# Kernel tuning notes

Measured on AMD Instinct MI355X. Metric: run time of the kernel, lower is better.

Reference implementation:

```python
import jax, jax.numpy as jnp
import numpy as np

N = 50000        # nodes
E = 400000       # edges (avg degree 8)
F_IN = 128       # num_features
HID = 64         # hidden_channels
H = 4            # num_heads
D = HID // H     # headc = 16
C = 16           # num_classes
K_HOPS = 3
ALPHA = 0.1
CST = 1e-5


def setup_inputs() -> dict:
    key = jax.random.key(0)
    ks = jax.random.split(key, 16)
    s = 0.05
    x = jax.random.normal(ks[0], (N, F_IN), dtype=jnp.float32)
    edge_index = jax.random.randint(ks[1], (2, E), 0, N, dtype=jnp.int64)
    Wi = jax.random.normal(ks[2], (F_IN, HID), dtype=jnp.float32) * s
    bi = jnp.zeros((HID,), dtype=jnp.float32)
    Wq = jax.random.normal(ks[3], (HID, H * D), dtype=jnp.float32) * s
    bq = jnp.zeros((H * D,), dtype=jnp.float32)
    Wk = jax.random.normal(ks[4], (HID, H * D), dtype=jnp.float32) * s
    bk = jnp.zeros((H * D,), dtype=jnp.float32)
    Wv = jax.random.normal(ks[5], (HID, H * C), dtype=jnp.float32) * s
    bv = jnp.zeros((H * C,), dtype=jnp.float32)
    Wo = jax.random.normal(ks[6], (H * C, C), dtype=jnp.float32) * s
    bo = jnp.zeros((C,), dtype=jnp.float32)
    # hopwise/temp init as in the torch module (ind_gamma=True, gamma_softmax=True)
    hw = ALPHA * (1.0 - ALPHA) ** np.arange(K_HOPS + 1)
    hw[-1] = (1.0 - ALPHA) ** K_HOPS
    hopwise = jnp.asarray(hw, dtype=jnp.float32)
    temp = jax.random.uniform(ks[7], (H, K_HOPS + 1), dtype=jnp.float32)
    return {"x": x, "edge_index": edge_index, "Wi": Wi, "bi": bi, "Wq": Wq,
            "bq": bq, "Wk": Wk, "bk": bk, "Wv": Wv, "bv": bv, "Wo": Wo,
            "bo": bo, "hopwise": hopwise, "temp": temp}


def reference(x, edge_index, Wi, bi, Wq, bq, Wk, bk, Wv, bv, Wo, bo, hopwise, temp):
    # dropout p=0 (inference); input transform + relu
    h = jax.nn.relu(x @ Wi + bi)                       # (N, HID)
    Q = (1.0 + jax.nn.elu(h @ Wq + bq)).reshape(N, H, D)
    Kt = (1.0 + jax.nn.elu(h @ Wk + bk)).reshape(N, H, D)
    V = (h @ Wv + bv).reshape(N, H, C)
    M = jnp.einsum('nhi,nhj->nhij', Kt, V)             # (N, H, D, C)
    hidden = V * temp[:, 0][None, :, None]             # hop-0 term
    # NB: torch F.softmax(temp, dim=-2) normalizes over the HEAD axis
    layerwise = jax.nn.softmax(temp, axis=0)           # (H, K+1)
    src, dst = edge_index[0], edge_index[1]
    for hop in range(K_HOPS):
        M = jax.ops.segment_sum(M[src], dst, num_segments=N)
        Kt = jax.ops.segment_sum(Kt[src], dst, num_segments=N)
        Hm = jnp.einsum('nhi,nhij->nhj', Q, M)         # (N, H, C)
        den = jnp.einsum('nhi,nhi->nh', Q, Kt)[..., None] + CST
        gamma = hopwise[hop + 1] * layerwise[:, hop + 1][:, None]  # (H, 1)
        hidden = hidden + gamma * (Hm / den)
    # multi_concat=True path
    out = hidden.reshape(N, H * C) @ Wo + bo           # (N, C)
    return out
```

## Files before the change

### kernel.cpp

```cpp
#include <hip/hip_runtime.h>
#include <math.h>

#define F_IN 128
#define HID  64
#define NH   4
#define DD   16
#define CC   16
#define CSTE 1e-5f

typedef _Float16 h2     __attribute__((ext_vector_type(2)));
typedef float    f2     __attribute__((ext_vector_type(2)));
typedef short    short8 __attribute__((ext_vector_type(8)));
typedef float    f4v    __attribute__((ext_vector_type(4)));

#define WIT_LD 136
#define W2T_LD 72
#define H_LD   72

__device__ __forceinline__ unsigned short bf16r(float f) {
    unsigned int u = __builtin_bit_cast(unsigned int, f);
    unsigned int r = (u + 0x7FFFu + ((u >> 16) & 1u)) >> 16;
    return (unsigned short)r;
}

__device__ __forceinline__ int uni(int v) {
    return __builtin_amdgcn_readfirstlane(v);
}

__device__ __forceinline__ float fp8_to_f32(unsigned int b) {
    f2 v = __builtin_amdgcn_cvt_pk_f32_fp8((int)b, false);
    return v.x;
}
__device__ __forceinline__ f2 fp8x2_to_f32(unsigned int w) {
    return __builtin_amdgcn_cvt_pk_f32_fp8((int)w, false);
}
__device__ __forceinline__ unsigned char f32_to_fp8(float f) {
    int w = __builtin_amdgcn_cvt_pk_fp8_f32(f, f, 0, false);
    return (unsigned char)(w & 0xff);
}

__device__ __forceinline__ float fp4_dec1(unsigned int n) {
    unsigned int e = (n >> 1) & 3u, m = n & 1u;
    float mag = (e == 0) ? 0.5f * (float)m
                         : (float)(1u << (e - 1)) * (1.0f + 0.5f * (float)m);
    return (n & 8u) ? -mag : mag;
}
__device__ __forceinline__ unsigned int fp4_enc1(float f) {
    unsigned int s = (f < 0.f) ? 8u : 0u;
    float a = fabsf(f);
    unsigned int m;
    if      (a < 0.25f) m = 0u;
    else if (a < 0.75f) m = 1u;
    else if (a < 1.25f) m = 2u;
    else if (a < 1.75f) m = 3u;
    else if (a < 2.5f)  m = 4u;
    else if (a < 3.5f)  m = 5u;
    else if (a < 5.0f)  m = 6u;
    else                m = 7u;
    return s | m;
}

#if __has_builtin(__builtin_amdgcn_cvt_scalef32_pk_f32_fp4) && __has_builtin(__builtin_amdgcn_cvt_scalef32_pk_fp4_f32)
#define HAS_FP4 1
#endif

__device__ __forceinline__ void fp4x16_dec2(uint2 w, f2* v) {
#ifdef HAS_FP4
    v[0] = __builtin_amdgcn_cvt_scalef32_pk_f32_fp4(w.x, 1.0f, 0);
    v[1] = __builtin_amdgcn_cvt_scalef32_pk_f32_fp4(w.x, 1.0f, 1);
    v[2] = __builtin_amdgcn_cvt_scalef32_pk_f32_fp4(w.x, 1.0f, 2);
    v[3] = __builtin_amdgcn_cvt_scalef32_pk_f32_fp4(w.x, 1.0f, 3);
    v[4] = __builtin_amdgcn_cvt_scalef32_pk_f32_fp4(w.y, 1.0f, 0);
    v[5] = __builtin_amdgcn_cvt_scalef32_pk_f32_fp4(w.y, 1.0f, 1);
    v[6] = __builtin_amdgcn_cvt_scalef32_pk_f32_fp4(w.y, 1.0f, 2);
    v[7] = __builtin_amdgcn_cvt_scalef32_pk_f32_fp4(w.y, 1.0f, 3);
#else
    #pragma unroll
    for (int j = 0; j < 4; ++j) {
        v[j].x     = fp4_dec1((w.x >> (8 * j)) & 0xFu);
        v[j].y     = fp4_dec1((w.x >> (8 * j + 4)) & 0xFu);
        v[4 + j].x = fp4_dec1((w.y >> (8 * j)) & 0xFu);
        v[4 + j].y = fp4_dec1((w.y >> (8 * j + 4)) & 0xFu);
    }
#endif
}

__device__ __forceinline__ uint2 fp4x16_enc(const float* v) {
#ifdef HAS_FP4
    unsigned int a = 0u, b = 0u;
    a = __builtin_amdgcn_cvt_scalef32_pk_fp4_f32(a, v[0],  v[1],  1.0f, 0);
    a = __builtin_amdgcn_cvt_scalef32_pk_fp4_f32(a, v[2],  v[3],  1.0f, 1);
    a = __builtin_amdgcn_cvt_scalef32_pk_fp4_f32(a, v[4],  v[5],  1.0f, 2);
    a = __builtin_amdgcn_cvt_scalef32_pk_fp4_f32(a, v[6],  v[7],  1.0f, 3);
    b = __builtin_amdgcn_cvt_scalef32_pk_fp4_f32(b, v[8],  v[9],  1.0f, 0);
    b = __builtin_amdgcn_cvt_scalef32_pk_fp4_f32(b, v[10], v[11], 1.0f, 1);
    b = __builtin_amdgcn_cvt_scalef32_pk_fp4_f32(b, v[12], v[13], 1.0f, 2);
    b = __builtin_amdgcn_cvt_scalef32_pk_fp4_f32(b, v[14], v[15], 1.0f, 3);
    return {a, b};
#else
    unsigned int a = 0u, b = 0u;
    #pragma unroll
    for (int j = 0; j < 8; ++j) {
        a |= fp4_enc1(v[j])     << (4 * j);
        b |= fp4_enc1(v[8 + j]) << (4 * j);
    }
    return {a, b};
#endif
}

__device__ __forceinline__ void store_m_row(
    uint2* __restrict__ Mout, unsigned short* __restrict__ SKout,
    int node, int lane, const float* u, float kacc)
{
    float rm = 0.f;
    #pragma unroll
    for (int j = 0; j < 16; ++j) rm = fmaxf(rm, fabsf(u[j]));
    unsigned char s8 = f32_to_fp8(rm * (1.0f / 6.0f));
    float se = fp8_to_f32((unsigned int)s8);
    float invs = (se > 0.f) ? (1.0f / se) : 0.f;
    float tq[16];
    #pragma unroll
    for (int j = 0; j < 16; ++j) tq[j] = u[j] * invs;
    Mout[(size_t)node * 64 + lane] = fp4x16_enc(tq);
    SKout[(size_t)node * 64 + lane] =
        (unsigned short)((unsigned short)s8 | ((unsigned short)f32_to_fp8(kacc) << 8));
}

__device__ __forceinline__ float gamma_for(const float* __restrict__ temp,
                                           const float* __restrict__ hopwise,
                                           int h, int hop) {
    float t0 = temp[0 * 4 + hop], t1 = temp[1 * 4 + hop];
    float t2 = temp[2 * 4 + hop], t3 = temp[3 * 4 + hop];
    float mx = fmaxf(fmaxf(t0, t1), fmaxf(t2, t3));
    float e0 = __expf(t0 - mx), e1 = __expf(t1 - mx);
    float e2 = __expf(t2 - mx), e3 = __expf(t3 - mx);
    float ssum = e0 + e1 + e2 + e3;
    float eh = (h == 0) ? e0 : (h == 1) ? e1 : (h == 2) ? e2 : e3;
    return hopwise[hop] * eh / ssum;
}

__device__ __forceinline__ void reduce_scatter16(float* u, int p) {
    #pragma unroll
    for (int k = 0; k < 4; ++k) {
        const int m = 1 << k;
        bool bit = (p >> k) & 1;
        const int n = 8 >> k;
        #pragma unroll
        for (int j = 0; j < n; ++j) {
            float give = bit ? u[2 * j]     : u[2 * j + 1];
            float keep = bit ? u[2 * j + 1] : u[2 * j];
            float got  = __shfl_xor(give, m, 64);
            u[j] = keep + got;
        }
    }
}

__device__ __forceinline__ float den16(float qd, float kacc) {
    float kq = qd * kacc;
    kq += __shfl_xor(kq, 1, 64);
    kq += __shfl_xor(kq, 2, 64);
    kq += __shfl_xor(kq, 4, 64);
    kq += __shfl_xor(kq, 8, 64);
    return kq + CSTE;
}

__device__ __forceinline__ void acc_edge23(f2* u2, float& kacc,
                                           uint2 w, unsigned int skraw) {
    f2 sk = fp8x2_to_f32(skraw);
    kacc += sk.y;
    f2 v[8];
    fp4x16_dec2(w, v);
    f2 s = {sk.x, sk.x};
    #pragma unroll
    for (int j = 0; j < 8; ++j) u2[j] = s * v[j] + u2[j];
}

__device__ __forceinline__ void acc_edge1(h2* u16, float& kacc,
                                          uint4 a0, uint4 a1, unsigned int kraw) {
    float kk = fp8_to_f32(kraw);
    kacc += kk;
    _Float16 kh = (_Float16)kk;
    h2 k2 = {kh, kh};
    const unsigned int aw[8] = {a0.x, a0.y, a0.z, a0.w, a1.x, a1.y, a1.z, a1.w};
    #pragma unroll
    for (int j = 0; j < 8; ++j)
        u16[j] += k2 * __builtin_bit_cast(h2, aw[j]);
}

__global__ __launch_bounds__(1024) void scan_a(const int* __restrict__ deg,
                                               int* __restrict__ offsets,
                                               int* __restrict__ bsum, int N) {
    __shared__ int wsum[16], woff[16];
    int lane = threadIdx.x & 63, w = threadIdx.x >> 6;
    int i0 = blockIdx.x * 4096 + (int)threadIdx.x * 4;
    int d0 = (i0 + 0 < N) ? deg[i0 + 0] : 0;
    int d1 = (i0 + 1 < N) ? deg[i0 + 1] : 0;
    int d2 = (i0 + 2 < N) ? deg[i0 + 2] : 0;
    int d3 = (i0 + 3 < N) ? deg[i0 + 3] : 0;
    int tsum = d0 + d1 + d2 + d3;
    int incl = tsum;
    #pragma unroll
    for (int m = 1; m < 64; m <<= 1) {
        int t = __shfl_up(incl, m, 64);
        if (lane >= m) incl += t;
    }
    if (lane == 63) wsum[w] = incl;
    __syncthreads();
    if (threadIdx.x == 0) {
        int r = 0;
        for (int k = 0; k < 16; ++k) { int t = wsum[k]; woff[k] = r; r += t; }
        bsum[blockIdx.x] = r;
    }
    __syncthreads();
    int excl = woff[w] + incl - tsum;
    if (i0 + 0 < N) offsets[i0 + 0] = excl;
    if (i0 + 1 < N) offsets[i0 + 1] = excl + d0;
    if (i0 + 2 < N) offsets[i0 + 2] = excl + d0 + d1;
    if (i0 + 3 < N) offsets[i0 + 3] = excl + d0 + d1 + d2;
}

__global__ void scan_c(int* __restrict__ offsets, const int* __restrict__ bsum,
                       int nb, int N) {
    int i = blockIdx.x * blockDim.x + threadIdx.x;
    if (i < N) {
        int bkt = i >> 12;
        int base = 0;
        for (int b = 0; b < bkt; ++b) base += bsum[b];
        offsets[i] += base;
    }
    if (i == 0) {
        int tot = 0;
        for (int b = 0; b < nb; ++b) tot += bsum[b];
        offsets[N] = tot;
    }
}

__global__ void scatter_kernel(const int* __restrict__ ei, const int* __restrict__ offsets,
                               int* __restrict__ cursor, int* __restrict__ csr, int E) {
    int e = blockIdx.x * blockDim.x + threadIdx.x;
    if (e < E) {
        int src = ei[e];
        int dst = ei[E + e];
        int pos = atomicAdd(&cursor[dst], 1);
        csr[offsets[dst] + pos] = src;
    }
}

__global__ __launch_bounds__(256) void qkv_count(
    const float* __restrict__ x,
    const float* __restrict__ Wi, const float* __restrict__ bi,
    const float* __restrict__ Wq, const float* __restrict__ bq,
    const float* __restrict__ Wk, const float* __restrict__ bk,
    const float* __restrict__ Wv, const float* __restrict__ bv,
    float* __restrict__ Q, unsigned char* __restrict__ K0,
    _Float16* __restrict__ Vh,
    const int* __restrict__ ei, int* __restrict__ deg,
    int E, int qb, int N)
{
    __shared__ unsigned short wit[64 * WIT_LD];
    __shared__ unsigned short w2t[192 * W2T_LD];
    __shared__ unsigned short hlds[64 * H_LD];
    if ((int)blockIdx.x >= qb) {
        int e = ((int)blockIdx.x - qb) * 256 + (int)threadIdx.x;
        if (e < E) atomicAdd(&deg[ei[E + e]], 1);
        return;
    }
    int t = threadIdx.x;
    #pragma unroll
    for (int i = 0; i < 32; ++i) {
        int g = t + i * 256;
        wit[(g & 63) * WIT_LD + (g >> 6)] = bf16r(Wi[g]);
    }
    #pragma unroll
    for (int i = 0; i < 16; ++i) {
        int g = t + i * 256;
        int k = g >> 6, n = g & 63;
        w2t[(n      ) * W2T_LD + k] = bf16r(Wq[g]);
        w2t[(n +  64) * W2T_LD + k] = bf16r(Wk[g]);
        w2t[(n + 128) * W2T_LD + k] = bf16r(Wv[g]);
    }
    __syncthreads();

    int lane = t & 63, w = t >> 6;
    int p = lane & 15, quad = lane >> 4;
    int mbase = blockIdx.x * 64 + w * 16;

    short8 afrag[4];
    {
        int node = mbase + p;
        if (node >= N) node = N - 1;
        const float* xr = x + (size_t)node * F_IN + quad * 8;
        #pragma unroll
        for (int ks = 0; ks < 4; ++ks) {
            float4 a0 = *(const float4*)(xr + ks * 32);
            float4 a1 = *(const float4*)(xr + ks * 32 + 4);
            short8 f;
            f[0] = bf16r(a0.x); f[1] = bf16r(a0.y); f[2] = bf16r(a0.z); f[3] = bf16r(a0.w);
            f[4] = bf16r(a1.x); f[5] = bf16r(a1.y); f[6] = bf16r(a1.z); f[7] = bf16r(a1.w);
            afrag[ks] = f;
        }
    }
    #pragma unroll
    for (int nt = 0; nt < 4; ++nt) {
        f4v acc = {0.f, 0.f, 0.f, 0.f};
        #pragma unroll
        for (int ks = 0; ks < 4; ++ks) {
            short8 b = *(const short8*)&wit[(nt * 16 + p) * WIT_LD + ks * 32 + quad * 8];
            acc = __builtin_amdgcn_mfma_f32_16x16x32_bf16(afrag[ks], b, acc, 0, 0, 0);
        }
        float bb = bi[nt * 16 + p];
        #pragma unroll
        for (int r = 0; r < 4; ++r) {
            float hv = fmaxf(acc[r] + bb, 0.f);
            hlds[(w * 16 + quad * 4 + r) * H_LD + nt * 16 + p] = bf16r(hv);
        }
    }
    __syncthreads();

    short8 ha0 = *(const short8*)&hlds[(w * 16 + p) * H_LD + quad * 8];
    short8 ha1 = *(const short8*)&hlds[(w * 16 + p) * H_LD + 32 + quad * 8];
    int node_r = mbase + quad * 4;
    #pragma unroll
    for (int nt = 0; nt < 12; ++nt) {
        f4v acc = {0.f, 0.f, 0.f, 0.f};
        short8 b0 = *(const short8*)&w2t[(nt * 16 + p) * W2T_LD + quad * 8];
        short8 b1 = *(const short8*)&w2t[(nt * 16 + p) * W2T_LD + 32 + quad * 8];
        acc = __builtin_amdgcn_mfma_f32_16x16x32_bf16(ha0, b0, acc, 0, 0, 0);
        acc = __builtin_amdgcn_mfma_f32_16x16x32_bf16(ha1, b1, acc, 0, 0, 0);
        int col = nt * 16 + p;
        #pragma unroll
        for (int r = 0; r < 4; ++r) {
            int node = node_r + r;
            if (node >= N) continue;
            float v = acc[r];
            if (col < 64) {
                v += bq[col];
                Q[(size_t)node * 64 + col] = (v > 0.f) ? (1.f + v) : __expf(v);
            } else if (col < 128) {
                int c = col - 64;
                v += bk[c];
                float kv = (v > 0.f) ? (1.f + v) : __expf(v);
                K0[(size_t)node * 64 + c] = f32_to_fp8(kv);
            } else {
                int c = col - 128;
                v += bv[c];
                Vh[(size_t)node * 64 + c] = (_Float16)v;
            }
        }
    }
}


__global__ __launch_bounds__(256) void hop1_all(
    const float* __restrict__ Q, const unsigned char* __restrict__ K0,
    const _Float16* __restrict__ Vh,
    const int* __restrict__ offsets, const int* __restrict__ csr,
    const float* __restrict__ temp, const float* __restrict__ hopwise,
    uint2* __restrict__ M1, unsigned short* __restrict__ SK1,
    float* __restrict__ hidden, int N)
{
    int lane = threadIdx.x & 63;
    int h = lane >> 4;
    float gh  = gamma_for(temp, hopwise, h, 1);
    float g0  = temp[h * 4];
    int wid    = blockIdx.x * 4 + (threadIdx.x >> 6);
    int nwaves = gridDim.x * 4;

    for (int node = wid; node < N; node += nwaves) {
        float h0 = (float)Vh[(size_t)node * 64 + lane] * g0;
        float qd = Q[(size_t)node * 64 + lane];
        h2 u16[8];
        #pragma unroll
        for (int j = 0; j < 8; ++j) u16[j] = h2{(_Float16)0.f, (_Float16)0.f};
        float kacc = 0.f;
        int beg = uni(offsets[node]), end = uni(offsets[node + 1]);
        int t = beg;
        for (; t + 3 < end; t += 4) {
            int s0 = uni(csr[t]),     s1 = uni(csr[t + 1]);
            int s2 = uni(csr[t + 2]), s3 = uni(csr[t + 3]);
            const uint4* v0p = (const uint4*)(Vh + (size_t)s0 * 64 + h * 16);
            const uint4* v1p = (const uint4*)(Vh + (size_t)s1 * 64 + h * 16);
            const uint4* v2p = (const uint4*)(Vh + (size_t)s2 * 64 + h * 16);
            const uint4* v3p = (const uint4*)(Vh + (size_t)s3 * 64 + h * 16);
            uint4 a00 = v0p[0], a01 = v0p[1];
            uint4 a10 = v1p[0], a11 = v1p[1];
            uint4 a20 = v2p[0], a21 = v2p[1];
            uint4 a30 = v3p[0], a31 = v3p[1];
            unsigned char k0 = K0[(size_t)s0 * 64 + lane];
            unsigned char k1 = K0[(size_t)s1 * 64 + lane];
            unsigned char k2 = K0[(size_t)s2 * 64 + lane];
            unsigned char k3 = K0[(size_t)s3 * 64 + lane];
            acc_edge1(u16, kacc, a00, a01, k0);
            acc_edge1(u16, kacc, a10, a11, k1);
            acc_edge1(u16, kacc, a20, a21, k2);
            acc_edge1(u16, kacc, a30, a31, k3);
        }
        for (; t < end; ++t) {
            int s = uni(csr[t]);
            const uint4* vp = (const uint4*)(Vh + (size_t)s * 64 + h * 16);
            uint4 a0 = vp[0], a1 = vp[1];
            unsigned char kk = K0[(size_t)s * 64 + lane];
            acc_edge1(u16, kacc, a0, a1, kk);
        }
        float u[16];
        #pragma unroll
        for (int j = 0; j < 8; ++j) { u[2 * j] = (float)u16[j].x; u[2 * j + 1] = (float)u16[j].y; }
        store_m_row(M1, SK1, node, lane, u, kacc);
        #pragma unroll
        for (int j = 0; j < 16; ++j) u[j] *= qd;
        reduce_scatter16(u, lane & 15);
        float g = gh / den16(qd, kacc);
        hidden[(size_t)node * 64 + lane] = h0 + g * u[0];
    }
}

template<bool STORE>
__global__ __launch_bounds__(256) void hop23_all(
    const float* __restrict__ Q, const uint2* __restrict__ Mprev,
    const unsigned short* __restrict__ SKprev,
    const int* __restrict__ offsets, const int* __restrict__ csr,
    const float* __restrict__ temp, const float* __restrict__ hopwise,
    uint2* __restrict__ Mnext, unsigned short* __restrict__ SKnext,
    float* __restrict__ hidden,
    const float* __restrict__ Wo, const float* __restrict__ bo,
    float* __restrict__ out, int N, int hop)
{
    int lane = threadIdx.x & 63;
    float gh = gamma_for(temp, hopwise, lane >> 4, hop);
    int wid    = blockIdx.x * 4 + (threadIdx.x >> 6);
    int nwaves = gridDim.x * 4;

    for (int node = wid; node < N; node += nwaves) {
        float qd  = Q[(size_t)node * 64 + lane];
        float hv0 = STORE ? 0.f : hidden[(size_t)node * 64 + lane];
        f2 u2[8];
        #pragma unroll
        for (int j = 0; j < 8; ++j) u2[j] = f2{0.f, 0.f};
        float kacc = 0.f;
        int beg = uni(offsets[node]), end = uni(offsets[node + 1]);
        int t = beg;
        for (; t + 3 < end; t += 4) {
            int s0 = uni(csr[t]),     s1 = uni(csr[t + 1]);
            int s2 = uni(csr[t + 2]), s3 = uni(csr[t + 3]);
            uint2 w0 = Mprev[(size_t)s0 * 64 + lane];
            uint2 w1 = Mprev[(size_t)s1 * 64 + lane];
            uint2 w2 = Mprev[(size_t)s2 * 64 + lane];
            uint2 w3 = Mprev[(size_t)s3 * 64 + lane];
            unsigned short k0 = SKprev[(size_t)s0 * 64 + lane];
            unsigned short k1 = SKprev[(size_t)s1 * 64 + lane];
            unsigned short k2 = SKprev[(size_t)s2 * 64 + lane];
            unsigned short k3 = SKprev[(size_t)s3 * 64 + lane];
            acc_edge23(u2, kacc, w0, k0);
            acc_edge23(u2, kacc, w1, k1);
            acc_edge23(u2, kacc, w2, k2);
            acc_edge23(u2, kacc, w3, k3);
        }
        for (; t < end; ++t) {
            int sn = uni(csr[t]);
            uint2 w = Mprev[(size_t)sn * 64 + lane];
            unsigned short skr = SKprev[(size_t)sn * 64 + lane];
            acc_edge23(u2, kacc, w, skr);
        }
        float u[16];
        #pragma unroll
        for (int j = 0; j < 8; ++j) { u[2 * j] = u2[j].x; u[2 * j + 1] = u2[j].y; }
        if constexpr (STORE) store_m_row(Mnext, SKnext, node, lane, u, kacc);
        #pragma unroll
        for (int j = 0; j < 16; ++j) u[j] *= qd;
        reduce_scatter16(u, lane & 15);
        float g = gh / den16(qd, kacc);
        if constexpr (STORE) {
            hidden[(size_t)node * 64 + lane] += g * u[0];
        } else {
            float wrow[16];
            {
                const f4v* wp = (const f4v*)(Wo + (size_t)lane * 16);
                f4v a = wp[0], b = wp[1], c = wp[2], d = wp[3];
                wrow[0]=a[0]; wrow[1]=a[1]; wrow[2]=a[2]; wrow[3]=a[3];
                wrow[4]=b[0]; wrow[5]=b[1]; wrow[6]=b[2]; wrow[7]=b[3];
                wrow[8]=c[0]; wrow[9]=c[1]; wrow[10]=c[2]; wrow[11]=c[3];
                wrow[12]=d[0]; wrow[13]=d[1]; wrow[14]=d[2]; wrow[15]=d[3];
            }
            float hv = hv0 + g * u[0];
            float o[16];
            #pragma unroll
            for (int j = 0; j < 16; ++j) o[j] = hv * wrow[j];
            reduce_scatter16(o, lane & 15);
            float r = o[0];
            r += __shfl_xor(r, 16, 64);
            r += __shfl_xor(r, 32, 64);
            if (lane < 16) out[(size_t)node * 16 + lane] = r + bo[lane];
        }
    }
}

extern "C" void kernel_launch(void* const* d_in, const int* in_sizes, int n_in,
                              void* d_out, int out_size, void* d_ws, size_t ws_size,
                              hipStream_t stream) {
    const float* x       = (const float*)d_in[0];
    const int*   ei      = (const int*)  d_in[1];
    const float* Wi      = (const float*)d_in[2];
    const float* bi      = (const float*)d_in[3];
    const float* Wq      = (const float*)d_in[4];
    const float* bq      = (const float*)d_in[5];
    const float* Wk      = (const float*)d_in[6];
    const float* bk      = (const float*)d_in[7];
    const float* Wv      = (const float*)d_in[8];
    const float* bv      = (const float*)d_in[9];
    const float* Wo      = (const float*)d_in[10];
    const float* bo      = (const float*)d_in[11];
    const float* hopwise = (const float*)d_in[12];
    const float* temp    = (const float*)d_in[13];

    const int N = in_sizes[0] / F_IN;
    const int E = in_sizes[1] / 2;

    char* ws = (char*)d_ws;
    size_t off = 0;
    auto take = [&](size_t bytes) -> char* {
        char* p = ws + off;
        off += (bytes + 255) & ~(size_t)255;
        return p;
    };
    float*          Q      = (float*)take((size_t)N * 64 * 4);
    _Float16*       Vh     = (_Float16*)take((size_t)N * 64 * 2);
    float*          hidden = (float*)take((size_t)N * 64 * 4);
    unsigned char*  K0     = (unsigned char*)take((size_t)N * 64);
    unsigned short* SK1    = (unsigned short*)take((size_t)N * 64 * 2);
    unsigned short* SK2    = (unsigned short*)take((size_t)N * 64 * 2);
    int*            degcur = (int*)take((size_t)2 * N * 4);
    int*            offs   = (int*)take((size_t)(N + 1) * 4);
    int*            csr    = (int*)take((size_t)E * 4);
    int             nb     = (N + 4095) / 4096;
    int*            bsum   = (int*)take((size_t)nb * 4);
    uint2*          M1     = (uint2*)take((size_t)N * 512);
    uint2*          M2     = (uint2*)take((size_t)N * 512);

    int* deg    = degcur;
    int* cursor = degcur + N;

    hipMemsetAsync(degcur, 0, (size_t)2 * N * 4, stream);

    int eb = (E + 255) / 256;
    int qb = (N + 63) / 64;
    qkv_count<<<qb + eb, 256, 0, stream>>>(x, Wi, bi, Wq, bq, Wk, bk, Wv, bv,
                                           Q, K0, Vh,
                                           ei, deg, E, qb, N);
    scan_a<<<nb, 1024, 0, stream>>>(deg, offs, bsum, N);
    scan_c<<<(N + 255) / 256, 256, 0, stream>>>(offs, bsum, nb, N);
    scatter_kernel<<<eb, 256, 0, stream>>>(ei, offs, cursor, csr, E);

    int nwb = (N + 3) / 4;
    int pgrid = nwb < 2048 ? nwb : 2048;
    hop1_all<<<pgrid, 256, 0, stream>>>(Q, K0, Vh, offs, csr, temp, hopwise,
                                        M1, SK1, hidden, N);
    hop23_all<true ><<<pgrid, 256, 0, stream>>>(Q, M1, SK1, offs, csr, temp, hopwise,
                                                M2, SK2, hidden,
                                                (const float*)nullptr, (const float*)nullptr,
                                                (float*)nullptr, N, 2);
    hop23_all<false><<<pgrid, 256, 0, stream>>>(Q, M2, SK2, offs, csr, temp, hopwise,
                                                (uint2*)nullptr, (unsigned short*)nullptr,
                                                hidden, Wo, bo, (float*)d_out, N, 3);
}
```

Measured before the change: 295.6 us.

## Pack fp8 V and K into one interleaved row and use one-node-per-wave grids

The projection kernel now also writes V as fp8, packed with the fp8 K into a single 128-byte row per node. Hop 1 then gathers one contiguous row per neighbour instead of separate fp16 V and fp8 K rows, and accumulates in fp32. This cuts the bytes and cache lines touched in the gather. All three hop kernels also drop the grid-stride loop in favour of one wave per node with a full-size grid, trading loop overhead for more block launches. The cost is lower V precision in hop 1 (fp8 instead of fp16) and one extra store in the projection kernel.

```diff
diff --git a/kernel.cpp b/kernel.cpp
--- a/kernel.cpp
+++ b/kernel.cpp
@@ -33,6 +33,9 @@
 }
 __device__ __forceinline__ f2 fp8x2_to_f32(unsigned int w) {
     return __builtin_amdgcn_cvt_pk_f32_fp8((int)w, false);
+}
+__device__ __forceinline__ f2 fp8x2_to_f32_hi(unsigned int w) {
+    return __builtin_amdgcn_cvt_pk_f32_fp8((int)w, true);
 }
 __device__ __forceinline__ unsigned char f32_to_fp8(float f) {
     int w = __builtin_amdgcn_cvt_pk_fp8_f32(f, f, 0, false);
@@ -175,16 +178,18 @@
     for (int j = 0; j < 8; ++j) u2[j] = s * v[j] + u2[j];
 }
 
-__device__ __forceinline__ void acc_edge1(h2* u16, float& kacc,
-                                          uint4 a0, uint4 a1, unsigned int kraw) {
+__device__ __forceinline__ void acc_edge1(f2* u2, float& kacc,
+                                          uint4 vw, unsigned int kraw) {
     float kk = fp8_to_f32(kraw);
     kacc += kk;
-    _Float16 kh = (_Float16)kk;
-    h2 k2 = {kh, kh};
-    const unsigned int aw[8] = {a0.x, a0.y, a0.z, a0.w, a1.x, a1.y, a1.z, a1.w};
-    #pragma unroll
-    for (int j = 0; j < 8; ++j)
-        u16[j] += k2 * __builtin_bit_cast(h2, aw[j]);
+    f2 v[8];
+    v[0] = fp8x2_to_f32(vw.x);  v[1] = fp8x2_to_f32_hi(vw.x);
+    v[2] = fp8x2_to_f32(vw.y);  v[3] = fp8x2_to_f32_hi(vw.y);
+    v[4] = fp8x2_to_f32(vw.z);  v[5] = fp8x2_to_f32_hi(vw.z);
+    v[6] = fp8x2_to_f32(vw.w);  v[7] = fp8x2_to_f32_hi(vw.w);
+    f2 s = {kk, kk};
+    #pragma unroll
+    for (int j = 0; j < 8; ++j) u2[j] = s * v[j] + u2[j];
 }
 
 __global__ __launch_bounds__(1024) void scan_a(const int* __restrict__ deg,
@@ -252,7 +257,7 @@
     const float* __restrict__ Wq, const float* __restrict__ bq,
     const float* __restrict__ Wk, const float* __restrict__ bk,
     const float* __restrict__ Wv, const float* __restrict__ bv,
-    float* __restrict__ Q, unsigned char* __restrict__ K0,
+    float* __restrict__ Q, unsigned char* __restrict__ VKq,
     _Float16* __restrict__ Vh,
     const int* __restrict__ ei, int* __restrict__ deg,
     int E, int qb, int N)
@@ -340,11 +345,12 @@
                 int c = col - 64;
                 v += bk[c];
                 float kv = (v > 0.f) ? (1.f + v) : __expf(v);
-                K0[(size_t)node * 64 + c] = f32_to_fp8(kv);
+                VKq[(size_t)node * 128 + 64 + c] = f32_to_fp8(kv);
             } else {
                 int c = col - 128;
                 v += bv[c];
                 Vh[(size_t)node * 64 + c] = (_Float16)v;
+                VKq[(size_t)node * 128 + c] = f32_to_fp8(v);
             }
         }
     }
@@ -352,7 +358,7 @@
 
 
 __global__ __launch_bounds__(256) void hop1_all(
-    const float* __restrict__ Q, const unsigned char* __restrict__ K0,
+    const float* __restrict__ Q, const unsigned char* __restrict__ VKq,
     const _Float16* __restrict__ Vh,
     const int* __restrict__ offsets, const int* __restrict__ csr,
     const float* __restrict__ temp, const float* __restrict__ hopwise,
@@ -360,58 +366,54 @@
     float* __restrict__ hidden, int N)
 {
     int lane = threadIdx.x & 63;
+    int node = blockIdx.x * 4 + (threadIdx.x >> 6);
+    if (node >= N) return;
     int h = lane >> 4;
-    float gh  = gamma_for(temp, hopwise, h, 1);
-    float g0  = temp[h * 4];
-    int wid    = blockIdx.x * 4 + (threadIdx.x >> 6);
-    int nwaves = gridDim.x * 4;
-
-    for (int node = wid; node < N; node += nwaves) {
-        float h0 = (float)Vh[(size_t)node * 64 + lane] * g0;
-        float qd = Q[(size_t)node * 64 + lane];
-        h2 u16[8];
-        #pragma unroll
-        for (int j = 0; j < 8; ++j) u16[j] = h2{(_Float16)0.f, (_Float16)0.f};
-        float kacc = 0.f;
-        int beg = uni(offsets[node]), end = uni(offsets[node + 1]);
-        int t = beg;
-        for (; t + 3 < end; t += 4) {
-            int s0 = uni(csr[t]),     s1 = uni(csr[t + 1]);
-            int s2 = uni(csr[t + 2]), s3 = uni(csr[t + 3]);
-            const uint4* v0p = (const uint4*)(Vh + (size_t)s0 * 64 + h * 16);
-            const uint4* v1p = (const uint4*)(Vh + (size_t)s1 * 64 + h * 16);
-            const uint4* v2p = (const uint4*)(Vh + (size_t)s2 * 64 + h * 16);
-            const uint4* v3p = (const uint4*)(Vh + (size_t)s3 * 64 + h * 16);
-            uint4 a00 = v0p[0], a01 = v0p[1];
-            uint4 a10 = v1p[0], a11 = v1p[1];
-            uint4 a20 = v2p[0], a21 = v2p[1];
-            uint4 a30 = v3p[0], a31 = v3p[1];
-            unsigned char k0 = K0[(size_t)s0 * 64 + lane];
-            unsigned char k1 = K0[(size_t)s1 * 64 + lane];
-            unsigned char k2 = K0[(size_t)s2 * 64 + lane];
-            unsigned char k3 = K0[(size_t)s3 * 64 + lane];
-            acc_edge1(u16, kacc, a00, a01, k0);
-            acc_edge1(u16, kacc, a10, a11, k1);
-            acc_edge1(u16, kacc, a20, a21, k2);
-            acc_edge1(u16, kacc, a30, a31, k3);
-        }
-        for (; t < end; ++t) {
-            int s = uni(csr[t]);
-            const uint4* vp = (const uint4*)(Vh + (size_t)s * 64 + h * 16);
-            uint4 a0 = vp[0], a1 = vp[1];
-            unsigned char kk = K0[(size_t)s * 64 + lane];
-            acc_edge1(u16, kacc, a0, a1, kk);
-        }
-        float u[16];
-        #pragma unroll
-        for (int j = 0; j < 8; ++j) { u[2 * j] = (float)u16[j].x; u[2 * j + 1] = (float)u16[j].y; }
-        store_m_row(M1, SK1, node, lane, u, kacc);
-        #pragma unroll
-        for (int j = 0; j < 16; ++j) u[j] *= qd;
-        reduce_scatter16(u, lane & 15);
-        float g = gh / den16(qd, kacc);
-        hidden[(size_t)node * 64 + lane] = h0 + g * u[0];
-    }
+    float gh = gamma_for(temp, hopwise, h, 1);
+    float h0 = (float)Vh[(size_t)node * 64 + lane] * temp[h * 4];
+    float qd = Q[(size_t)node * 64 + lane];
+    f2 u2[8];
+    #pragma unroll
+    for (int j = 0; j < 8; ++j) u2[j] = f2{0.f, 0.f};
+    float kacc = 0.f;
+    int beg = uni(offsets[node]), end = uni(offsets[node + 1]);
+    int t = beg;
+    for (; t + 3 < end; t += 4) {
+        int s0 = uni(csr[t]),     s1 = uni(csr[t + 1]);
+        int s2 = uni(csr[t + 2]), s3 = uni(csr[t + 3]);
+        const unsigned char* b0 = VKq + (size_t)s0 * 128;
+        const unsigned char* b1 = VKq + (size_t)s1 * 128;
+        const unsigned char* b2 = VKq + (size_t)s2 * 128;
+        const unsigned char* b3 = VKq + (size_t)s3 * 128;
+        uint4 v0 = *(const uint4*)(b0 + h * 16);
+        uint4 v1 = *(const uint4*)(b1 + h * 16);
+        uint4 v2 = *(const uint4*)(b2 + h * 16);
+        uint4 v3 = *(const uint4*)(b3 + h * 16);
+        unsigned char k0 = b0[64 + lane];
+        unsigned char k1 = b1[64 + lane];
+        unsigned char k2 = b2[64 + lane];
+        unsigned char k3 = b3[64 + lane];
+        acc_edge1(u2, kacc, v0, k0);
+        acc_edge1(u2, kacc, v1, k1);
+        acc_edge1(u2, kacc, v2, k2);
+        acc_edge1(u2, kacc, v3, k3);
+    }
+    for (; t < end; ++t) {
+        int s = uni(csr[t]);
+        const unsigned char* b = VKq + (size_t)s * 128;
+        uint4 vw = *(const uint4*)(b + h * 16);
+        unsigned char kk = b[64 + lane];
+        acc_edge1(u2, kacc, vw, kk);
+    }
+    float u[16];
+    #pragma unroll
+    for (int j = 0; j < 8; ++j) { u[2 * j] = u2[j].x; u[2 * j + 1] = u2[j].y; }
+    store_m_row(M1, SK1, node, lane, u, kacc);
+    #pragma unroll
+    for (int j = 0; j < 16; ++j) u[j] *= qd;
+    reduce_scatter16(u, lane & 15);
+    float g = gh / den16(qd, kacc);
+    hidden[(size_t)node * 64 + lane] = h0 + g * u[0];
 }
 
 template<bool STORE>
@@ -426,71 +428,68 @@
     float* __restrict__ out, int N, int hop)
 {
     int lane = threadIdx.x & 63;
+    int node = blockIdx.x * 4 + (threadIdx.x >> 6);
+    if (node >= N) return;
     float gh = gamma_for(temp, hopwise, lane >> 4, hop);
-    int wid    = blockIdx.x * 4 + (threadIdx.x >> 6);
-    int nwaves = gridDim.x * 4;
-
-    for (int node = wid; node < N; node += nwaves) {
-        float qd  = Q[(size_t)node * 64 + lane];
-        float hv0 = STORE ? 0.f : hidden[(size_t)node * 64 + lane];
-        f2 u2[8];
+    float qd  = Q[(size_t)node * 64 + lane];
+    float hv0 = STORE ? 0.f : hidden[(size_t)node * 64 + lane];
+    f2 u2[8];
+    #pragma unroll
+    for (int j = 0; j < 8; ++j) u2[j] = f2{0.f, 0.f};
+    float kacc = 0.f;
+    int beg = uni(offsets[node]), end = uni(offsets[node + 1]);
+    int t = beg;
+    for (; t + 3 < end; t += 4) {
+        int s0 = uni(csr[t]),     s1 = uni(csr[t + 1]);
+        int s2 = uni(csr[t + 2]), s3 = uni(csr[t + 3]);
+        uint2 w0 = Mprev[(size_t)s0 * 64 + lane];
+        uint2 w1 = Mprev[(size_t)s1 * 64 + lane];
+        uint2 w2 = Mprev[(size_t)s2 * 64 + lane];
+        uint2 w3 = Mprev[(size_t)s3 * 64 + lane];
+        unsigned short k0 = SKprev[(size_t)s0 * 64 + lane];
+        unsigned short k1 = SKprev[(size_t)s1 * 64 + lane];
+        unsigned short k2 = SKprev[(size_t)s2 * 64 + lane];
+        unsigned short k3 = SKprev[(size_t)s3 * 64 + lane];
+        acc_edge23(u2, kacc, w0, k0);
+        acc_edge23(u2, kacc, w1, k1);
+        acc_edge23(u2, kacc, w2, k2);
+        acc_edge23(u2, kacc, w3, k3);
+    }
+    for (; t < end; ++t) {
+        int sn = uni(csr[t]);
+        uint2 w = Mprev[(size_t)sn * 64 + lane];
+        unsigned short skr = SKprev[(size_t)sn * 64 + lane];
+        acc_edge23(u2, kacc, w, skr);
+    }
+    float u[16];
+    #pragma unroll
+    for (int j = 0; j < 8; ++j) { u[2 * j] = u2[j].x; u[2 * j + 1] = u2[j].y; }
+    if constexpr (STORE) store_m_row(Mnext, SKnext, node, lane, u, kacc);
+    #pragma unroll
+    for (int j = 0; j < 16; ++j) u[j] *= qd;
+    reduce_scatter16(u, lane & 15);
+    float g = gh / den16(qd, kacc);
+    if constexpr (STORE) {
+        hidden[(size_t)node * 64 + lane] += g * u[0];
+    } else {
+        float wrow[16];
+        {
+            const f4v* wp = (const f4v*)(Wo + (size_t)lane * 16);
+            f4v a = wp[0], b = wp[1], c = wp[2], d = wp[3];
+            wrow[0]=a[0]; wrow[1]=a[1]; wrow[2]=a[2]; wrow[3]=a[3];
+            wrow[4]=b[0]; wrow[5]=b[1]; wrow[6]=b[2]; wrow[7]=b[3];
+            wrow[8]=c[0]; wrow[9]=c[1]; wrow[10]=c[2]; wrow[11]=c[3];
+            wrow[12]=d[0]; wrow[13]=d[1]; wrow[14]=d[2]; wrow[15]=d[3];
+        }
+        float hv = hv0 + g * u[0];
+        float o[16];
         #pragma unroll
-        for (int j = 0; j < 8; ++j) u2[j] = f2{0.f, 0.f};
-        float kacc = 0.f;
-        int beg = uni(offsets[node]), end = uni(offsets[node + 1]);
-        int t = beg;
-        for (; t + 3 < end; t += 4) {
-            int s0 = uni(csr[t]),     s1 = uni(csr[t + 1]);
-            int s2 = uni(csr[t + 2]), s3 = uni(csr[t + 3]);
-            uint2 w0 = Mprev[(size_t)s0 * 64 + lane];
-            uint2 w1 = Mprev[(size_t)s1 * 64 + lane];
-            uint2 w2 = Mprev[(size_t)s2 * 64 + lane];
-            uint2 w3 = Mprev[(size_t)s3 * 64 + lane];
-            unsigned short k0 = SKprev[(size_t)s0 * 64 + lane];
-            unsigned short k1 = SKprev[(size_t)s1 * 64 + lane];
-            unsigned short k2 = SKprev[(size_t)s2 * 64 + lane];
-            unsigned short k3 = SKprev[(size_t)s3 * 64 + lane];
-            acc_edge23(u2, kacc, w0, k0);
-            acc_edge23(u2, kacc, w1, k1);
-            acc_edge23(u2, kacc, w2, k2);
-            acc_edge23(u2, kacc, w3, k3);
-        }
-        for (; t < end; ++t) {
-            int sn = uni(csr[t]);
-            uint2 w = Mprev[(size_t)sn * 64 + lane];
-            unsigned short skr = SKprev[(size_t)sn * 64 + lane];
-            acc_edge23(u2, kacc, w, skr);
-        }
-        float u[16];
-        #pragma unroll
-        for (int j = 0; j < 8; ++j) { u[2 * j] = u2[j].x; u[2 * j + 1] = u2[j].y; }
-        if constexpr (STORE) store_m_row(Mnext, SKnext, node, lane, u, kacc);
-        #pragma unroll
-        for (int j = 0; j < 16; ++j) u[j] *= qd;
-        reduce_scatter16(u, lane & 15);
-        float g = gh / den16(qd, kacc);
-        if constexpr (STORE) {
-            hidden[(size_t)node * 64 + lane] += g * u[0];
-        } else {
-            float wrow[16];
-            {
-                const f4v* wp = (const f4v*)(Wo + (size_t)lane * 16);
-                f4v a = wp[0], b = wp[1], c = wp[2], d = wp[3];
-                wrow[0]=a[0]; wrow[1]=a[1]; wrow[2]=a[2]; wrow[3]=a[3];
-                wrow[4]=b[0]; wrow[5]=b[1]; wrow[6]=b[2]; wrow[7]=b[3];
-                wrow[8]=c[0]; wrow[9]=c[1]; wrow[10]=c[2]; wrow[11]=c[3];
-                wrow[12]=d[0]; wrow[13]=d[1]; wrow[14]=d[2]; wrow[15]=d[3];
-            }
-            float hv = hv0 + g * u[0];
-            float o[16];
-            #pragma unroll
-            for (int j = 0; j < 16; ++j) o[j] = hv * wrow[j];
-            reduce_scatter16(o, lane & 15);
-            float r = o[0];
-            r += __shfl_xor(r, 16, 64);
-            r += __shfl_xor(r, 32, 64);
-            if (lane < 16) out[(size_t)node * 16 + lane] = r + bo[lane];
-        }
+        for (int j = 0; j < 16; ++j) o[j] = hv * wrow[j];
+        reduce_scatter16(o, lane & 15);
+        float r = o[0];
+        r += __shfl_xor(r, 16, 64);
+        r += __shfl_xor(r, 32, 64);
+        if (lane < 16) out[(size_t)node * 16 + lane] = r + bo[lane];
     }
 }
 
@@ -525,7 +524,7 @@
     float*          Q      = (float*)take((size_t)N * 64 * 4);
     _Float16*       Vh     = (_Float16*)take((size_t)N * 64 * 2);
     float*          hidden = (float*)take((size_t)N * 64 * 4);
-    unsigned char*  K0     = (unsigned char*)take((size_t)N * 64);
+    unsigned char*  VKq    = (unsigned char*)take((size_t)N * 128);
     unsigned short* SK1    = (unsigned short*)take((size_t)N * 64 * 2);
     unsigned short* SK2    = (unsigned short*)take((size_t)N * 64 * 2);
     int*            degcur = (int*)take((size_t)2 * N * 4);
@@ -544,21 +543,20 @@
     int eb = (E + 255) / 256;
     int qb = (N + 63) / 64;
     qkv_count<<<qb + eb, 256, 0, stream>>>(x, Wi, bi, Wq, bq, Wk, bk, Wv, bv,
-                                           Q, K0, Vh,
+                                           Q, VKq, Vh,
                                            ei, deg, E, qb, N);
     scan_a<<<nb, 1024, 0, stream>>>(deg, offs, bsum, N);
     scan_c<<<(N + 255) / 256, 256, 0, stream>>>(offs, bsum, nb, N);
     scatter_kernel<<<eb, 256, 0, stream>>>(ei, offs, cursor, csr, E);
 
-    int nwb = (N + 3) / 4;
-    int pgrid = nwb < 2048 ? nwb : 2048;
-    hop1_all<<<pgrid, 256, 0, stream>>>(Q, K0, Vh, offs, csr, temp, hopwise,
-                                        M1, SK1, hidden, N);
-    hop23_all<true ><<<pgrid, 256, 0, stream>>>(Q, M1, SK1, offs, csr, temp, hopwise,
-                                                M2, SK2, hidden,
-                                                (const float*)nullptr, (const float*)nullptr,
-                                                (float*)nullptr, N, 2);
-    hop23_all<false><<<pgrid, 256, 0, stream>>>(Q, M2, SK2, offs, csr, temp, hopwise,
-                                                (uint2*)nullptr, (unsigned short*)nullptr,
-                                                hidden, Wo, bo, (float*)d_out, N, 3);
-}
+    int nb4 = (N + 3) / 4;
+    hop1_all<<<nb4, 256, 0, stream>>>(Q, VKq, Vh, offs, csr, temp, hopwise,
+                                      M1, SK1, hidden, N);
+    hop23_all<true ><<<nb4, 256, 0, stream>>>(Q, M1, SK1, offs, csr, temp, hopwise,
+                                              M2, SK2, hidden,
+                                              (const float*)nullptr, (const float*)nullptr,
+                                              (float*)nullptr, N, 2);
+    hop23_all<false><<<nb4, 256, 0, stream>>>(Q, M2, SK2, offs, csr, temp, hopwise,
+                                              (uint2*)nullptr, (unsigned short*)nullptr,
+                                              hidden, Wo, bo, (float*)d_out, N, 3);
+}
```

After: 288.7 us. -2.3%, faster.
